# Kernel tuning notes

Hardware: AMD Instinct MI355X
Metric: run time of the kernel (lower is better)

## Reference

```python
import jax, jax.numpy as jnp
import numpy as np
import math

B, S, E, H = 2, 2048, 1024, 16
D = E // H
# neuromodulator levels (deterministic branch choices)
NA, ACH, DA = 0.5, 0.5, -0.5

def setup_inputs() -> dict:
    key = jax.random.key(0)
    ks = jax.random.split(key, 12)
    xav = lambda k, i, o: jax.random.uniform(k, (i, o), jnp.float32, -1.0, 1.0) * math.sqrt(6.0 / (i + o))
    return {
        'query': jax.random.normal(ks[0], (B, S, E), jnp.float32),
        'key':   jax.random.normal(ks[1], (B, S, E), jnp.float32),
        'value': jax.random.normal(ks[2], (B, S, E), jnp.float32),
        'Wq': xav(ks[3], E, E), 'bq': jnp.zeros((E,), jnp.float32),
        'Wk': xav(ks[4], E, E), 'bk': jnp.zeros((E,), jnp.float32),
        'Wv': xav(ks[5], E, E), 'bv': jnp.zeros((E,), jnp.float32),
        'Wo': xav(ks[6], E, E), 'bo': jnp.zeros((E,), jnp.float32),
        'time_scales': jnp.ones((H,), jnp.float32),
    }

def reference(query, key, value, Wq, bq, Wk, bk, Wv, bv, Wo, bo, time_scales):
    # projections -> [B, H, S, D]
    q = (query @ Wq + bq).reshape(B, S, H, D).transpose(0, 2, 1, 3)
    k = (key   @ Wk + bk).reshape(B, S, H, D).transpose(0, 2, 1, 3)
    v = (value @ Wv + bv).reshape(B, S, H, D).transpose(0, 2, 1, 3)
    # per-head time-scale on keys
    k = k * time_scales[None, :, None, None]
    scores = jnp.einsum('bhtd,bhsd->bhts', q, k) / math.sqrt(D)
    # noradrenaline: temperature scaling
    temperature = 1.0 / (1.0 + NA * 0.5)
    scores = scores / temperature
    # acetylcholine: boost diagonal
    diag = jnp.eye(S, dtype=scores.dtype)[None, None]
    scores = scores * (1.0 + ACH * 0.3 * diag)
    kk = max(1, int(S * 0.2))
    topv = jax.lax.top_k(scores, kk)[0]          # [B,H,S,kk]
    min_topk = topv[..., -1:]                     # kth largest
    mask = (scores >= min_topk).astype(scores.dtype)
    scores = scores * (1.0 + (-DA) * 0.3 * mask)
    attn = jax.nn.softmax(scores, axis=-1)
    out = jnp.einsum('bhts,bhsd->bhtd', attn, v)
    out = out.transpose(0, 2, 1, 3).reshape(B, S, E)
    out = out @ Wo + bo
    return out
```

## Files before the change

kernel.cpp:

```cpp
#include <hip/hip_runtime.h>
#include <cstdint>
#include <cstddef>

#define BB 2
#define SS 2048
#define EE 1024
#define HH 16
#define DH 64
#define KKSEL 409
#define QT 16
#define PST 136

typedef __attribute__((ext_vector_type(8))) short bf16x8;
typedef __attribute__((ext_vector_type(4))) float f32x4;
typedef unsigned short ushort_t;

__device__ __forceinline__ unsigned short f2bf(float f){
    unsigned u = __float_as_uint(f);
    u += 0x7fffu + ((u >> 16) & 1u);
    return (unsigned short)(u >> 16);
}
__device__ __forceinline__ float bf2f(unsigned short h){
    return __uint_as_float(((unsigned)h) << 16);
}
__device__ __forceinline__ unsigned sortkey(float f){
    unsigned u = __float_as_uint(f);
    return (u & 0x80000000u) ? ~u : (u | 0x80000000u);
}
__device__ __forceinline__ float inv_sortkey(unsigned k){
    unsigned u = (k & 0x80000000u) ? (k & 0x7fffffffu) : ~k;
    return __uint_as_float(u);
}
__device__ __forceinline__ void split8(const float* f, bf16x8& h, bf16x8& l){
    #pragma unroll
    for (int j = 0; j < 8; ++j){
        ushort_t hh = f2bf(f[j]);
        h[j] = (short)hh;
        l[j] = (short)f2bf(f[j] - bf2f(hh));
    }
}
__device__ __forceinline__ void gload_lds16(const ushort_t* g, ushort_t* l){
    __builtin_amdgcn_global_load_lds(
        (const __attribute__((address_space(1))) void*)g,
        (__attribute__((address_space(3))) void*)l, 16, 0, 0);
}

__device__ __forceinline__ float topk_thresh(const float* cand){
    float mx = cand[0], mn = cand[0];
    #pragma unroll
    for (int j = 1; j < 32; ++j){
        mx = fmaxf(mx, cand[j]);
        mn = fminf(mn, cand[j]);
    }
    #pragma unroll
    for (int off = 1; off < 64; off <<= 1){
        mx = fmaxf(mx, __shfl_xor(mx, off, 64));
        mn = fminf(mn, __shfl_xor(mn, off, 64));
    }
    unsigned lo = sortkey(mn), hi = sortkey(mx) + 1u;
    #pragma unroll 1
    for (int it = 0; it < 32 && (hi - lo) > 1u; ++it){
        const unsigned mid = lo + ((hi - lo) >> 1);
        const float midf = inv_sortkey(mid);
        int c = 0;
        #pragma unroll
        for (int j = 0; j < 32; ++j)
            c += (int)__popcll(__ballot(cand[j] >= midf));
        if (c == KKSEL){ lo = mid; break; }
        if (c > KKSEL) lo = mid; else hi = mid;
    }
    return inv_sortkey(lo);
}

struct CvtArgs {
    const float* W[4];
    ushort_t* H[4];
    ushort_t* L[4];
};

__global__ __launch_bounds__(256) void convert_wt4(CvtArgs a)
{
    __shared__ float T[64][65];
    const int z = blockIdx.z;
    const float* __restrict__ W = a.W[z];
    ushort_t* __restrict__ Ht = a.H[z];
    ushort_t* __restrict__ Lt = a.L[z];

    const int tid = threadIdx.x;
    const int ty = tid >> 4, tx = tid & 15;
    const int n0 = blockIdx.x * 64, k0 = blockIdx.y * 64;
    #pragma unroll
    for (int i = 0; i < 4; ++i){
        const int kl = ty + i * 16;
        float4 w = *(const float4*)&W[(size_t)(k0 + kl) * EE + n0 + tx * 4];
        T[kl][tx*4 + 0] = w.x; T[kl][tx*4 + 1] = w.y;
        T[kl][tx*4 + 2] = w.z; T[kl][tx*4 + 3] = w.w;
    }
    __syncthreads();
    #pragma unroll
    for (int i = 0; i < 4; ++i){
        const int nl = ty + i * 16;
        ushort4 h, l;
        ushort_t* hp = &h.x; ushort_t* lp = &l.x;
        #pragma unroll
        for (int j = 0; j < 4; ++j){
            const float v = T[tx*4 + j][nl];
            ushort_t hh = f2bf(v);
            hp[j] = hh;
            lp[j] = f2bf(v - bf2f(hh));
        }
        const size_t o = (size_t)(n0 + nl) * EE + k0 + tx * 4;
        *(ushort4*)&Ht[o] = h;
        *(ushort4*)&Lt[o] = l;
    }
}

template<int MODE>
__device__ __forceinline__ void gemm_body(
        const float* __restrict__ X,
        const ushort_t* __restrict__ Wth, const ushort_t* __restrict__ Wtl,
        const float* __restrict__ bias, const float* __restrict__ ts,
        float* __restrict__ OutF, ushort_t* __restrict__ OutH,
        ushort_t* __restrict__ OutL, ushort_t* buf)
{
    const int tid  = threadIdx.x;
    const int lane = tid & 63, wave = tid >> 6;
    const int c16  = lane & 15, qd = lane >> 4;
    const int m0 = blockIdx.y * 128, n0 = blockIdx.x * 128;
    const int wm = (wave >> 1) * 64, wn = (wave & 1) * 64;
    const int lrow = tid >> 1, lkg = (tid & 1) * 16;

    f32x4 acc[4][4];
    #pragma unroll
    for (int a = 0; a < 4; ++a)
        #pragma unroll
        for (int b = 0; b < 4; ++b) acc[a][b] = (f32x4){0.f,0.f,0.f,0.f};

    const float* Xr = X + (size_t)(m0 + lrow) * EE + lkg;

    const int seg0 = wave * 2, seg1 = wave * 2 + 1;
    const size_t wofs0 = (size_t)(n0 + seg0*16 + (lane >> 2)) * EE + (lane & 3) * 8;
    const size_t wofs1 = (size_t)(n0 + seg1*16 + (lane >> 2)) * EE + (lane & 3) * 8;
    const ushort_t* WhA = Wth + wofs0;
    const ushort_t* WhB = Wth + wofs1;
    const ushort_t* WlA = Wtl + wofs0;
    const ushort_t* WlB = Wtl + wofs1;

    {
        ushort_t* S = buf;
        gload_lds16(WhA, S + 8192  + seg0*512);
        gload_lds16(WhB, S + 8192  + seg1*512);
        gload_lds16(WlA, S + 12288 + seg0*512);
        gload_lds16(WlB, S + 12288 + seg1*512);
        float fx[16];
        *(float4*)&fx[0]  = *(const float4*)&Xr[0];
        *(float4*)&fx[4]  = *(const float4*)&Xr[4];
        *(float4*)&fx[8]  = *(const float4*)&Xr[8];
        *(float4*)&fx[12] = *(const float4*)&Xr[12];
        bf16x8 h0, l0, h1, l1;
        split8(fx, h0, l0); split8(fx + 8, h1, l1);
        *(bf16x8*)&S[lrow*32 + lkg]           = h0;
        *(bf16x8*)&S[lrow*32 + lkg + 8]       = h1;
        *(bf16x8*)&S[4096 + lrow*32 + lkg]    = l0;
        *(bf16x8*)&S[4096 + lrow*32 + lkg+8]  = l1;
    }
    __syncthreads();

    int cur = 0;
    for (int k0 = 0; k0 < EE; k0 += 32){
        const bool more = (k0 + 32) < EE;
        float fx[16];
        if (more){
            const int kt = k0 + 32;
            ushort_t* N = buf + (cur ^ 1) * 16384;
            gload_lds16(WhA + kt, N + 8192  + seg0*512);
            gload_lds16(WhB + kt, N + 8192  + seg1*512);
            gload_lds16(WlA + kt, N + 12288 + seg0*512);
            gload_lds16(WlB + kt, N + 12288 + seg1*512);
            const float* xp = Xr + kt;
            *(float4*)&fx[0]  = *(const float4*)&xp[0];
            *(float4*)&fx[4]  = *(const float4*)&xp[4];
            *(float4*)&fx[8]  = *(const float4*)&xp[8];
            *(float4*)&fx[12] = *(const float4*)&xp[12];
        }
        const ushort_t* S  = buf + cur * 16384;
        const ushort_t* A0 = S;
        const ushort_t* A1 = S + 4096;
        const ushort_t* B0 = S + 8192;
        const ushort_t* B1 = S + 12288;
        bf16x8 afh[4], afl[4], bfh[4], bfl[4];
        #pragma unroll
        for (int i = 0; i < 4; ++i){
            afh[i] = *(const bf16x8*)&A0[(wm + i*16 + c16)*32 + qd*8];
            afl[i] = *(const bf16x8*)&A1[(wm + i*16 + c16)*32 + qd*8];
            bfh[i] = *(const bf16x8*)&B0[(wn + i*16 + c16)*32 + qd*8];
            bfl[i] = *(const bf16x8*)&B1[(wn + i*16 + c16)*32 + qd*8];
        }
        #pragma unroll
        for (int a = 0; a < 4; ++a){
            #pragma unroll
            for (int b = 0; b < 4; ++b){
                if (MODE == 2){
                    acc[a][b] = __builtin_amdgcn_mfma_f32_16x16x32_bf16(afh[a], bfh[b], acc[a][b], 0,0,0);
                    acc[a][b] = __builtin_amdgcn_mfma_f32_16x16x32_bf16(afh[a], bfl[b], acc[a][b], 0,0,0);
                    acc[a][b] = __builtin_amdgcn_mfma_f32_16x16x32_bf16(afl[a], bfh[b], acc[a][b], 0,0,0);
                } else {
                    acc[a][b] = __builtin_amdgcn_mfma_f32_16x16x32_bf16(bfh[a], afh[b], acc[a][b], 0,0,0);
                    acc[a][b] = __builtin_amdgcn_mfma_f32_16x16x32_bf16(bfh[a], afl[b], acc[a][b], 0,0,0);
                    acc[a][b] = __builtin_amdgcn_mfma_f32_16x16x32_bf16(bfl[a], afh[b], acc[a][b], 0,0,0);
                }
            }
        }
        if (more){
            bf16x8 h0, l0, h1, l1;
            split8(fx, h0, l0); split8(fx + 8, h1, l1);
            ushort_t* N = buf + (cur ^ 1) * 16384;
            *(bf16x8*)&N[lrow*32 + lkg]           = h0;
            *(bf16x8*)&N[lrow*32 + lkg + 8]       = h1;
            *(bf16x8*)&N[4096 + lrow*32 + lkg]    = l0;
            *(bf16x8*)&N[4096 + lrow*32 + lkg+8]  = l1;
            __syncthreads();
            cur ^= 1;
        }
    }

    if (MODE == 3){
        #pragma unroll
        for (int a = 0; a < 4; ++a){
            const int ng = n0 + wn + a*16 + qd*4;
            float4 b4 = *(const float4*)&bias[ng];
            const float bb[4] = {b4.x, b4.y, b4.z, b4.w};
            #pragma unroll
            for (int b = 0; b < 4; ++b){
                const int mg = m0 + wm + b*16 + c16;
                float4 o;
                o.x = acc[a][b][0] + bb[0]; o.y = acc[a][b][1] + bb[1];
                o.z = acc[a][b][2] + bb[2]; o.w = acc[a][b][3] + bb[3];
                *(float4*)&OutF[(size_t)mg * EE + ng] = o;
            }
        }
    } else if (MODE == 0){
        #pragma unroll
        for (int a = 0; a < 4; ++a){
            const int ng = n0 + wn + a*16 + qd*4;
            const int h = ng >> 6, d0 = ng & 63;
            float4 b4 = *(const float4*)&bias[ng];
            const float bb[4] = {b4.x, b4.y, b4.z, b4.w};
            #pragma unroll
            for (int b = 0; b < 4; ++b){
                const int mg = m0 + wm + b*16 + c16;
                const int bi = mg >> 11, s = mg & (SS - 1);
                ushort4 hv, lv;
                ushort_t* hp = &hv.x; ushort_t* lp = &lv.x;
                #pragma unroll
                for (int r = 0; r < 4; ++r){
                    const float v = (acc[a][b][r] + bb[r]) * 0.15625f;
                    ushort_t hh = f2bf(v);
                    hp[r] = hh;
                    lp[r] = f2bf(v - bf2f(hh));
                }
                const size_t o = (((size_t)(bi * HH + h)) * SS + s) * DH + d0;
                *(ushort4*)&OutH[o] = hv;
                *(ushort4*)&OutL[o] = lv;
            }
        }
    } else if (MODE == 1){
        #pragma unroll
        for (int a = 0; a < 4; ++a){
            const int ng = n0 + wn + a*16 + qd*4;
            const int h = ng >> 6, d0 = ng & 63;
            const float tsc = ts[h];
            float4 b4 = *(const float4*)&bias[ng];
            const float bb[4] = {b4.x, b4.y, b4.z, b4.w};
            #pragma unroll
            for (int b = 0; b < 4; ++b){
                const int mg = m0 + wm + b*16 + c16;
                const int bi = mg >> 11, s = mg & (SS - 1);
                ushort4 hv;
                ushort_t* hp = &hv.x;
                #pragma unroll
                for (int r = 0; r < 4; ++r)
                    hp[r] = f2bf((acc[a][b][r] + bb[r]) * tsc);
                *(ushort4*)&OutH[(((size_t)(bi * HH + h)) * SS + s) * DH + d0] = hv;
            }
        }
    } else {
        #pragma unroll
        for (int a = 0; a < 4; ++a){
            const int mg = m0 + wm + a*16 + qd*4;
            const int bi = mg >> 11, s0 = mg & (SS - 1);
            #pragma unroll
            for (int b = 0; b < 4; ++b){
                const int ng = n0 + wn + b*16 + c16;
                const int h = ng >> 6, d = ng & 63;
                const float bv = bias[ng];
                ushort4 hv;
                ushort_t* hp = &hv.x;
                #pragma unroll
                for (int r = 0; r < 4; ++r) hp[r] = f2bf(acc[a][b][r] + bv);
                *(ushort4*)&OutH[(((size_t)(bi * HH + h)) * DH + d) * SS + s0] = hv;
            }
        }
    }
}

__global__ __launch_bounds__(256) void gemm_qkv(
        const float* __restrict__ q, const float* __restrict__ k,
        const float* __restrict__ v,
        const ushort_t* __restrict__ Wqh, const ushort_t* __restrict__ Wql,
        const ushort_t* __restrict__ Wkh, const ushort_t* __restrict__ Wkl,
        const ushort_t* __restrict__ Wvh, const ushort_t* __restrict__ Wvl,
        const float* __restrict__ bq, const float* __restrict__ bk,
        const float* __restrict__ bv, const float* __restrict__ ts,
        ushort_t* __restrict__ Qh, ushort_t* __restrict__ Ql,
        ushort_t* __restrict__ Kh, ushort_t* __restrict__ Vth)
{
    __shared__ ushort_t buf[2 * 16384];
    const int z = blockIdx.z;
    if (z == 0)
        gemm_body<0>(q, Wqh, Wql, bq, nullptr, nullptr, Qh, Ql, buf);
    else if (z == 1)
        gemm_body<1>(k, Wkh, Wkl, bk, ts, nullptr, Kh, nullptr, buf);
    else
        gemm_body<2>(v, Wvh, Wvl, bv, nullptr, nullptr, Vth, nullptr, buf);
}

__global__ __launch_bounds__(256) void gemm_out(
        const float* __restrict__ X,
        const ushort_t* __restrict__ Wth, const ushort_t* __restrict__ Wtl,
        const float* __restrict__ bias, float* __restrict__ OutF)
{
    __shared__ ushort_t buf[2 * 16384];
    gemm_body<3>(X, Wth, Wtl, bias, nullptr, OutF, nullptr, nullptr, buf);
}

__global__ __launch_bounds__(512, 4) void attn_kernel(
        const ushort_t* __restrict__ Qh, const ushort_t* __restrict__ Ql,
        const ushort_t* __restrict__ Khi, const ushort_t* __restrict__ Vth,
        float* __restrict__ AO)
{
    __shared__ __align__(16) char uni[65536];
    __shared__ float wsums[8][16];
    __shared__ float thr16[16];

    const int tid  = threadIdx.x;
    const int lane = tid & 63;
    const int wave = tid >> 6;
    const int qd   = lane >> 4;
    const int c16  = lane & 15;
    const unsigned Bx = blockIdx.x;
    const int xcd  = Bx & 7;
    const int qq   = Bx >> 3;
    const int tile = qq & 127;
    const int bh   = (qq >> 7) * 8 + xcd;
    const int t0   = tile * QT;
    const int wbase = wave * 256;

    bf16x8 qh[2], ql[2];
    {
        const size_t qbase = ((size_t)bh * SS + t0 + c16) * DH;
        #pragma unroll
        for (int kc = 0; kc < 2; ++kc){
            qh[kc] = *(const bf16x8*)&Qh[qbase + kc*32 + qd*8];
            ql[kc] = *(const bf16x8*)&Ql[qbase + kc*32 + qd*8];
        }
    }

    f32x4 acc[16];
    const ushort_t* Kh = Khi + (size_t)bh * SS * DH;
    #pragma unroll
    for (int t = 0; t < 16; ++t){
        f32x4 a = {0.f, 0.f, 0.f, 0.f};
        const int srow = wbase + t*16 + c16;
        const ushort_t* kp = Kh + (size_t)srow * DH + qd*8;
        #pragma unroll
        for (int kc = 0; kc < 2; ++kc){
            bf16x8 kh = *(const bf16x8*)(kp + kc*32);
            a = __builtin_amdgcn_mfma_f32_16x16x32_bf16(qh[kc], kh, a, 0, 0, 0);
            a = __builtin_amdgcn_mfma_f32_16x16x32_bf16(ql[kc], kh, a, 0, 0, 0);
        }
        acc[t] = a;
    }

    if (wave == (t0 >> 8)){
        #pragma unroll
        for (int t = 0; t < 16; ++t){
            const int colg = wbase + t*16 + c16;
            #pragma unroll
            for (int r = 0; r < 4; ++r)
                if (colg == t0 + qd*4 + r) acc[t][r] *= 1.15f;
        }
    }

    float* ex = (float*)uni;
    if (qd < 2){
        const int rl = (qd & 1) * 4;
        #pragma unroll
        for (int t = 0; t < 16; ++t)
            #pragma unroll
            for (int r = 0; r < 4; ++r)
                ex[(rl + r) * SS + wbase + t*16 + c16] = acc[t][r];
    }
    __syncthreads();
    float cand[32];
    #pragma unroll
    for (int j = 0; j < 32; ++j)
        cand[j] = ex[wave * SS + lane + 64*j];
    __syncthreads();
    if (qd >= 2){
        const int rl = (qd & 1) * 4;
        #pragma unroll
        for (int t = 0; t < 16; ++t)
            #pragma unroll
            for (int r = 0; r < 4; ++r)
                ex[(rl + r) * SS + wbase + t*16 + c16] = acc[t][r];
    }
    {
        const float th0 = topk_thresh(cand);
        if (lane == 0) thr16[wave] = th0;
    }
    __syncthreads();
    #pragma unroll
    for (int j = 0; j < 32; ++j)
        cand[j] = ex[wave * SS + lane + 64*j];
    {
        const float th1 = topk_thresh(cand);
        if (lane == 0) thr16[8 + wave] = th1;
    }
    __syncthreads();

    float thr[4];
    #pragma unroll
    for (int r = 0; r < 4; ++r) thr[r] = thr16[qd*4 + r];
    float psum[4] = {0.f, 0.f, 0.f, 0.f};
    #pragma unroll
    for (int t = 0; t < 16; ++t){
        #pragma unroll
        for (int r = 0; r < 4; ++r){
            const float s = acc[t][r];
            const float m = (s >= thr[r]) ? 1.15f : 1.0f;
            const float e = __expf(s * m);
            acc[t][r] = e;
            psum[r] += e;
        }
    }
    #pragma unroll
    for (int off = 1; off <= 8; off <<= 1){
        #pragma unroll
        for (int r = 0; r < 4; ++r) psum[r] += __shfl_xor(psum[r], off, 64);
    }
    if (c16 == 0){
        #pragma unroll
        for (int r = 0; r < 4; ++r) wsums[wave][qd*4 + r] = psum[r];
    }
    __syncthreads();
    float pinv[4];
    #pragma unroll
    for (int r = 0; r < 4; ++r){
        const int row = qd*4 + r;
        float s = 0.f;
        #pragma unroll
        for (int w = 0; w < 8; ++w) s += wsums[w][row];
        pinv[r] = 1.f / s;
    }

    const ushort_t* Vh = Vth + (size_t)bh * DH * SS;
    ushort_t* pw = (ushort_t*)uni + wave * (QT * PST);
    f32x4 oacc[4];
    #pragma unroll
    for (int dt = 0; dt < 4; ++dt) oacc[dt] = (f32x4){0.f, 0.f, 0.f, 0.f};

    #pragma unroll
    for (int half = 0; half < 2; ++half){
        #pragma unroll
        for (int tt = 0; tt < 8; ++tt){
            const int t = half*8 + tt;
            #pragma unroll
            for (int r = 0; r < 4; ++r)
                pw[(qd*4 + r) * PST + tt*16 + c16] = f2bf(acc[t][r] * pinv[r]);
        }
        #pragma unroll
        for (int kc = 0; kc < 4; ++kc){
            bf16x8 pf = *(const bf16x8*)&pw[c16 * PST + kc*32 + qd*8];
            const int sbase = wbase + half*128 + kc*32 + qd*8;
            #pragma unroll
            for (int dt = 0; dt < 4; ++dt){
                const int d = dt*16 + c16;
                bf16x8 vh = *(const bf16x8*)(Vh + (size_t)d * SS + sbase);
                oacc[dt] = __builtin_amdgcn_mfma_f32_16x16x32_bf16(pf, vh, oacc[dt], 0, 0, 0);
            }
        }
    }

    __syncthreads();
    float* red = (float*)uni;
    #pragma unroll
    for (int dt = 0; dt < 4; ++dt)
        #pragma unroll
        for (int r = 0; r < 4; ++r)
            red[(wave*16 + qd*4 + r) * 65 + dt*16 + c16] = oacc[dt][r];
    __syncthreads();

    const int b = bh >> 4, h = bh & 15;
    {
        const int r  = tid >> 5;
        const int c2 = (tid & 31) * 2;
        float s0 = 0.f, s1 = 0.f;
        #pragma unroll
        for (int w = 0; w < 8; ++w){
            s0 += red[(w*16 + r) * 65 + c2];
            s1 += red[(w*16 + r) * 65 + c2 + 1];
        }
        float2 o; o.x = s0; o.y = s1;
        *(float2*)&AO[((size_t)b * SS + t0 + r) * EE + h*DH + c2] = o;
    }
}

extern "C" void kernel_launch(void* const* d_in, const int* in_sizes, int n_in,
                              void* d_out, int out_size, void* d_ws, size_t ws_size,
                              hipStream_t stream)
{
    const float* query = (const float*)d_in[0];
    const float* key   = (const float*)d_in[1];
    const float* value = (const float*)d_in[2];
    const float* Wq    = (const float*)d_in[3];
    const float* bq    = (const float*)d_in[4];
    const float* Wk    = (const float*)d_in[5];
    const float* bk    = (const float*)d_in[6];
    const float* Wv    = (const float*)d_in[7];
    const float* bv    = (const float*)d_in[8];
    const float* Wo    = (const float*)d_in[9];
    const float* bo    = (const float*)d_in[10];
    const float* ts    = (const float*)d_in[11];
    float* out = (float*)d_out;
    char* w = (char*)d_ws;

    const size_t MB = 1u << 20;
    ushort_t* Qh  = (ushort_t*)(w + 0 * MB);
    ushort_t* Ql  = (ushort_t*)(w + 8 * MB);
    ushort_t* Kh  = (ushort_t*)(w + 16 * MB);
    ushort_t* Vth = (ushort_t*)(w + 24 * MB);
    float*    AOw = (float*)   (w + 32 * MB);
    ushort_t* Wqh = (ushort_t*)(w + 32 * MB);
    ushort_t* Wql = (ushort_t*)(w + 34 * MB);
    ushort_t* Wkh = (ushort_t*)(w + 36 * MB);
    ushort_t* Wkl = (ushort_t*)(w + 38 * MB);
    ushort_t* Wvh = (ushort_t*)(w + 40 * MB);
    ushort_t* Wvl = (ushort_t*)(w + 42 * MB);
    ushort_t* Woh = (ushort_t*)(w + 48 * MB);
    ushort_t* Wol = (ushort_t*)(w + 50 * MB);

    CvtArgs ca;
    ca.W[0] = Wq;  ca.W[1] = Wk;  ca.W[2] = Wv;  ca.W[3] = Wo;
    ca.H[0] = Wqh; ca.H[1] = Wkh; ca.H[2] = Wvh; ca.H[3] = Woh;
    ca.L[0] = Wql; ca.L[1] = Wkl; ca.L[2] = Wvl; ca.L[3] = Wol;

    hipLaunchKernelGGL(convert_wt4, dim3(16, 16, 4), dim3(256), 0, stream, ca);
    hipLaunchKernelGGL(gemm_qkv, dim3(8, 32, 3), dim3(256), 0, stream,
                       query, key, value, Wqh, Wql, Wkh, Wkl, Wvh, Wvl,
                       bq, bk, bv, ts, Qh, Ql, Kh, Vth);
    hipLaunchKernelGGL(attn_kernel, dim3(BB * HH * (SS / QT)), dim3(512), 0, stream,
                       Qh, Ql, Kh, Vth, AOw);
    hipLaunchKernelGGL(gemm_out, dim3(8, 32), dim3(256), 0, stream,
                       AOw, Woh, Wol, bo, out);
}
```

Baseline: 671.5 us.

## Pre-split activations to bf16 hi/lo and stage GEMM A tiles via direct LDS loads

```diff
diff --git a/kernel.cpp b/kernel.cpp
--- a/kernel.cpp
+++ b/kernel.cpp
@@ -45,8 +45,8 @@
         (__attribute__((address_space(3))) void*)l, 16, 0, 0);
 }
 
-__device__ __forceinline__ float topk_thresh(const float* cand){
-    float mx = cand[0], mn = cand[0];
+__device__ __forceinline__ void wave_minmax(const float* cand, float& mn, float& mx){
+    mx = cand[0]; mn = cand[0];
     #pragma unroll
     for (int j = 1; j < 32; ++j){
         mx = fmaxf(mx, cand[j]);
@@ -57,6 +57,8 @@
         mx = fmaxf(mx, __shfl_xor(mx, off, 64));
         mn = fminf(mn, __shfl_xor(mn, off, 64));
     }
+}
+__device__ __forceinline__ float bisect_thresh(const float* cand, float mn, float mx){
     unsigned lo = sortkey(mn), hi = sortkey(mx) + 1u;
     #pragma unroll 1
     for (int it = 0; it < 32 && (hi - lo) > 1u; ++it){
@@ -115,9 +117,31 @@
     }
 }
 
+struct CvtX {
+    const float* X[3];
+    ushort_t* H[3];
+    ushort_t* L[3];
+};
+
+__global__ __launch_bounds__(256) void convert_x3(CvtX a)
+{
+    const int z = blockIdx.z;
+    const float* __restrict__ X = a.X[z];
+    ushort_t* __restrict__ Hd = a.H[z];
+    ushort_t* __restrict__ Ld = a.L[z];
+    const size_t i = ((size_t)blockIdx.x * 256 + threadIdx.x) * 8;
+    float fx[8];
+    *(float4*)&fx[0] = *(const float4*)&X[i];
+    *(float4*)&fx[4] = *(const float4*)&X[i + 4];
+    bf16x8 h, l;
+    split8(fx, h, l);
+    *(bf16x8*)&Hd[i] = h;
+    *(bf16x8*)&Ld[i] = l;
+}
+
 template<int MODE>
 __device__ __forceinline__ void gemm_body(
-        const float* __restrict__ X,
+        const ushort_t* __restrict__ Xh, const ushort_t* __restrict__ Xl,
         const ushort_t* __restrict__ Wth, const ushort_t* __restrict__ Wtl,
         const float* __restrict__ bias, const float* __restrict__ ts,
         float* __restrict__ OutF, ushort_t* __restrict__ OutH,
@@ -128,7 +152,6 @@
     const int c16  = lane & 15, qd = lane >> 4;
     const int m0 = blockIdx.y * 128, n0 = blockIdx.x * 128;
     const int wm = (wave >> 1) * 64, wn = (wave & 1) * 64;
-    const int lrow = tid >> 1, lkg = (tid & 1) * 16;
 
     f32x4 acc[4][4];
     #pragma unroll
@@ -136,53 +159,31 @@
         #pragma unroll
         for (int b = 0; b < 4; ++b) acc[a][b] = (f32x4){0.f,0.f,0.f,0.f};
 
-    const float* Xr = X + (size_t)(m0 + lrow) * EE + lkg;
-
-    const int seg0 = wave * 2, seg1 = wave * 2 + 1;
-    const size_t wofs0 = (size_t)(n0 + seg0*16 + (lane >> 2)) * EE + (lane & 3) * 8;
-    const size_t wofs1 = (size_t)(n0 + seg1*16 + (lane >> 2)) * EE + (lane & 3) * 8;
-    const ushort_t* WhA = Wth + wofs0;
-    const ushort_t* WhB = Wth + wofs1;
-    const ushort_t* WlA = Wtl + wofs0;
-    const ushort_t* WlB = Wtl + wofs1;
-
-    {
-        ushort_t* S = buf;
-        gload_lds16(WhA, S + 8192  + seg0*512);
-        gload_lds16(WhB, S + 8192  + seg1*512);
-        gload_lds16(WlA, S + 12288 + seg0*512);
-        gload_lds16(WlB, S + 12288 + seg1*512);
-        float fx[16];
-        *(float4*)&fx[0]  = *(const float4*)&Xr[0];
-        *(float4*)&fx[4]  = *(const float4*)&Xr[4];
-        *(float4*)&fx[8]  = *(const float4*)&Xr[8];
-        *(float4*)&fx[12] = *(const float4*)&Xr[12];
-        bf16x8 h0, l0, h1, l1;
-        split8(fx, h0, l0); split8(fx + 8, h1, l1);
-        *(bf16x8*)&S[lrow*32 + lkg]           = h0;
-        *(bf16x8*)&S[lrow*32 + lkg + 8]       = h1;
-        *(bf16x8*)&S[4096 + lrow*32 + lkg]    = l0;
-        *(bf16x8*)&S[4096 + lrow*32 + lkg+8]  = l1;
-    }
+    const int seg0 = wave * 2, seg1 = seg0 + 1;
+    const int rl = lane >> 2, kl = (lane & 3) * 8;
+    const size_t aofs0 = (size_t)(m0 + seg0*16 + rl) * EE + kl;
+    const size_t aofs1 = (size_t)(m0 + seg1*16 + rl) * EE + kl;
+    const size_t bofs0 = (size_t)(n0 + seg0*16 + rl) * EE + kl;
+    const size_t bofs1 = (size_t)(n0 + seg1*16 + rl) * EE + kl;
+
+    auto stage = [&](ushort_t* S, int kt){
+        gload_lds16(Xh  + aofs0 + kt, S +         seg0*512);
+        gload_lds16(Xh  + aofs1 + kt, S +         seg1*512);
+        gload_lds16(Xl  + aofs0 + kt, S + 4096  + seg0*512);
+        gload_lds16(Xl  + aofs1 + kt, S + 4096  + seg1*512);
+        gload_lds16(Wth + bofs0 + kt, S + 8192  + seg0*512);
+        gload_lds16(Wth + bofs1 + kt, S + 8192  + seg1*512);
+        gload_lds16(Wtl + bofs0 + kt, S + 12288 + seg0*512);
+        gload_lds16(Wtl + bofs1 + kt, S + 12288 + seg1*512);
+    };
+
+    stage(buf, 0);
     __syncthreads();
 
     int cur = 0;
     for (int k0 = 0; k0 < EE; k0 += 32){
         const bool more = (k0 + 32) < EE;
-        float fx[16];
-        if (more){
-            const int kt = k0 + 32;
-            ushort_t* N = buf + (cur ^ 1) * 16384;
-            gload_lds16(WhA + kt, N + 8192  + seg0*512);
-            gload_lds16(WhB + kt, N + 8192  + seg1*512);
-            gload_lds16(WlA + kt, N + 12288 + seg0*512);
-            gload_lds16(WlB + kt, N + 12288 + seg1*512);
-            const float* xp = Xr + kt;
-            *(float4*)&fx[0]  = *(const float4*)&xp[0];
-            *(float4*)&fx[4]  = *(const float4*)&xp[4];
-            *(float4*)&fx[8]  = *(const float4*)&xp[8];
-            *(float4*)&fx[12] = *(const float4*)&xp[12];
-        }
+        if (more) stage(buf + (cur ^ 1) * 16384, k0 + 32);
         const ushort_t* S  = buf + cur * 16384;
         const ushort_t* A0 = S;
         const ushort_t* A1 = S + 4096;
@@ -212,13 +213,6 @@
             }
         }
         if (more){
-            bf16x8 h0, l0, h1, l1;
-            split8(fx, h0, l0); split8(fx + 8, h1, l1);
-            ushort_t* N = buf + (cur ^ 1) * 16384;
-            *(bf16x8*)&N[lrow*32 + lkg]           = h0;
-            *(bf16x8*)&N[lrow*32 + lkg + 8]       = h1;
-            *(bf16x8*)&N[4096 + lrow*32 + lkg]    = l0;
-            *(bf16x8*)&N[4096 + lrow*32 + lkg+8]  = l1;
             __syncthreads();
             cur ^= 1;
         }
@@ -305,8 +299,9 @@
 }
 
 __global__ __launch_bounds__(256) void gemm_qkv(
-        const float* __restrict__ q, const float* __restrict__ k,
-        const float* __restrict__ v,
+        const ushort_t* __restrict__ Xqh, const ushort_t* __restrict__ Xql,
+        const ushort_t* __restrict__ Xkh, const ushort_t* __restrict__ Xkl,
+        const ushort_t* __restrict__ Xvh, const ushort_t* __restrict__ Xvl,
         const ushort_t* __restrict__ Wqh, const ushort_t* __restrict__ Wql,
         const ushort_t* __restrict__ Wkh, const ushort_t* __restrict__ Wkl,
         const ushort_t* __restrict__ Wvh, const ushort_t* __restrict__ Wvl,
@@ -318,26 +313,26 @@
     __shared__ ushort_t buf[2 * 16384];
     const int z = blockIdx.z;
     if (z == 0)
-        gemm_body<0>(q, Wqh, Wql, bq, nullptr, nullptr, Qh, Ql, buf);
+        gemm_body<0>(Xqh, Xql, Wqh, Wql, bq, nullptr, nullptr, Qh, Ql, buf);
     else if (z == 1)
-        gemm_body<1>(k, Wkh, Wkl, bk, ts, nullptr, Kh, nullptr, buf);
+        gemm_body<1>(Xkh, Xkl, Wkh, Wkl, bk, ts, nullptr, Kh, nullptr, buf);
     else
-        gemm_body<2>(v, Wvh, Wvl, bv, nullptr, nullptr, Vth, nullptr, buf);
+        gemm_body<2>(Xvh, Xvl, Wvh, Wvl, bv, nullptr, nullptr, Vth, nullptr, buf);
 }
 
 __global__ __launch_bounds__(256) void gemm_out(
-        const float* __restrict__ X,
+        const ushort_t* __restrict__ AOh, const ushort_t* __restrict__ AOl,
         const ushort_t* __restrict__ Wth, const ushort_t* __restrict__ Wtl,
         const float* __restrict__ bias, float* __restrict__ OutF)
 {
     __shared__ ushort_t buf[2 * 16384];
-    gemm_body<3>(X, Wth, Wtl, bias, nullptr, OutF, nullptr, nullptr, buf);
+    gemm_body<3>(AOh, AOl, Wth, Wtl, bias, nullptr, OutF, nullptr, nullptr, buf);
 }
 
 __global__ __launch_bounds__(512, 4) void attn_kernel(
         const ushort_t* __restrict__ Qh, const ushort_t* __restrict__ Ql,
         const ushort_t* __restrict__ Khi, const ushort_t* __restrict__ Vth,
-        float* __restrict__ AO)
+        ushort_t* __restrict__ AOh, ushort_t* __restrict__ AOl)
 {
     __shared__ __align__(16) char uni[65536];
     __shared__ float wsums[8][16];
@@ -407,16 +402,18 @@
     for (int j = 0; j < 32; ++j)
         cand[j] = ex[wave * SS + lane + 64*j];
     __syncthreads();
-    if (qd >= 2){
-        const int rl = (qd & 1) * 4;
-        #pragma unroll
-        for (int t = 0; t < 16; ++t)
-            #pragma unroll
-            for (int r = 0; r < 4; ++r)
-                ex[(rl + r) * SS + wbase + t*16 + c16] = acc[t][r];
-    }
     {
-        const float th0 = topk_thresh(cand);
+        float mn, mx;
+        wave_minmax(cand, mn, mx);
+        if (qd >= 2){
+            const int rl = (qd & 1) * 4;
+            #pragma unroll
+            for (int t = 0; t < 16; ++t)
+                #pragma unroll
+                for (int r = 0; r < 4; ++r)
+                    ex[(rl + r) * SS + wbase + t*16 + c16] = acc[t][r];
+        }
+        const float th0 = bisect_thresh(cand, mn, mx);
         if (lane == 0) thr16[wave] = th0;
     }
     __syncthreads();
@@ -424,7 +421,9 @@
     for (int j = 0; j < 32; ++j)
         cand[j] = ex[wave * SS + lane + 64*j];
     {
-        const float th1 = topk_thresh(cand);
+        float mn, mx;
+        wave_minmax(cand, mn, mx);
+        const float th1 = bisect_thresh(cand, mn, mx);
         if (lane == 0) thr16[8 + wave] = th1;
     }
     __syncthreads();
@@ -466,29 +465,42 @@
 
     const ushort_t* Vh = Vth + (size_t)bh * DH * SS;
     ushort_t* pw = (ushort_t*)uni + wave * (QT * PST);
+
+    #pragma unroll
+    for (int tt = 0; tt < 8; ++tt)
+        #pragma unroll
+        for (int r = 0; r < 4; ++r)
+            pw[(qd*4 + r) * PST + tt*16 + c16] = f2bf(acc[tt][r] * pinv[r]);
+
     f32x4 oacc[4];
     #pragma unroll
     for (int dt = 0; dt < 4; ++dt) oacc[dt] = (f32x4){0.f, 0.f, 0.f, 0.f};
 
     #pragma unroll
-    for (int half = 0; half < 2; ++half){
-        #pragma unroll
-        for (int tt = 0; tt < 8; ++tt){
-            const int t = half*8 + tt;
-            #pragma unroll
-            for (int r = 0; r < 4; ++r)
-                pw[(qd*4 + r) * PST + tt*16 + c16] = f2bf(acc[t][r] * pinv[r]);
-        }
-        #pragma unroll
-        for (int kc = 0; kc < 4; ++kc){
-            bf16x8 pf = *(const bf16x8*)&pw[c16 * PST + kc*32 + qd*8];
-            const int sbase = wbase + half*128 + kc*32 + qd*8;
-            #pragma unroll
-            for (int dt = 0; dt < 4; ++dt){
-                const int d = dt*16 + c16;
-                bf16x8 vh = *(const bf16x8*)(Vh + (size_t)d * SS + sbase);
-                oacc[dt] = __builtin_amdgcn_mfma_f32_16x16x32_bf16(pf, vh, oacc[dt], 0, 0, 0);
-            }
+    for (int kc = 0; kc < 4; ++kc){
+        bf16x8 pf = *(const bf16x8*)&pw[c16 * PST + kc*32 + qd*8];
+        const int sbase = wbase + kc*32 + qd*8;
+        #pragma unroll
+        for (int dt = 0; dt < 4; ++dt){
+            const int d = dt*16 + c16;
+            bf16x8 vh = *(const bf16x8*)(Vh + (size_t)d * SS + sbase);
+            oacc[dt] = __builtin_amdgcn_mfma_f32_16x16x32_bf16(pf, vh, oacc[dt], 0, 0, 0);
+        }
+    }
+    #pragma unroll
+    for (int tt = 0; tt < 8; ++tt)
+        #pragma unroll
+        for (int r = 0; r < 4; ++r)
+            pw[(qd*4 + r) * PST + tt*16 + c16] = f2bf(acc[8 + tt][r] * pinv[r]);
+    #pragma unroll
+    for (int kc = 0; kc < 4; ++kc){
+        bf16x8 pf = *(const bf16x8*)&pw[c16 * PST + kc*32 + qd*8];
+        const int sbase = wbase + 128 + kc*32 + qd*8;
+        #pragma unroll
+        for (int dt = 0; dt < 4; ++dt){
+            const int d = dt*16 + c16;
+            bf16x8 vh = *(const bf16x8*)(Vh + (size_t)d * SS + sbase);
+            oacc[dt] = __builtin_amdgcn_mfma_f32_16x16x32_bf16(pf, vh, oacc[dt], 0, 0, 0);
         }
     }
 
@@ -511,8 +523,12 @@
             s0 += red[(w*16 + r) * 65 + c2];
             s1 += red[(w*16 + r) * 65 + c2 + 1];
         }
-        float2 o; o.x = s0; o.y = s1;
-        *(float2*)&AO[((size_t)b * SS + t0 + r) * EE + h*DH + c2] = o;
+        const size_t o = ((size_t)b * SS + t0 + r) * EE + h*DH + c2;
+        ushort2 hv, lv;
+        hv.x = f2bf(s0); lv.x = f2bf(s0 - bf2f(hv.x));
+        hv.y = f2bf(s1); lv.y = f2bf(s1 - bf2f(hv.y));
+        *(ushort2*)&AOh[o] = hv;
+        *(ushort2*)&AOl[o] = lv;
     }
 }
 
@@ -540,27 +556,41 @@
     ushort_t* Ql  = (ushort_t*)(w + 8 * MB);
     ushort_t* Kh  = (ushort_t*)(w + 16 * MB);
     ushort_t* Vth = (ushort_t*)(w + 24 * MB);
-    float*    AOw = (float*)   (w + 32 * MB);
     ushort_t* Wqh = (ushort_t*)(w + 32 * MB);
     ushort_t* Wql = (ushort_t*)(w + 34 * MB);
     ushort_t* Wkh = (ushort_t*)(w + 36 * MB);
     ushort_t* Wkl = (ushort_t*)(w + 38 * MB);
     ushort_t* Wvh = (ushort_t*)(w + 40 * MB);
     ushort_t* Wvl = (ushort_t*)(w + 42 * MB);
-    ushort_t* Woh = (ushort_t*)(w + 48 * MB);
-    ushort_t* Wol = (ushort_t*)(w + 50 * MB);
+    ushort_t* Woh = (ushort_t*)(w + 44 * MB);
+    ushort_t* Wol = (ushort_t*)(w + 46 * MB);
+    ushort_t* Xqh = (ushort_t*)(w + 48 * MB);
+    ushort_t* Xql = (ushort_t*)(w + 56 * MB);
+    ushort_t* Xkh = (ushort_t*)(w + 64 * MB);
+    ushort_t* Xkl = (ushort_t*)(w + 72 * MB);
+    ushort_t* Xvh = (ushort_t*)(w + 80 * MB);
+    ushort_t* Xvl = (ushort_t*)(w + 88 * MB);
+    ushort_t* AOh = (ushort_t*)(w + 48 * MB);
+    ushort_t* AOl = (ushort_t*)(w + 56 * MB);
 
     CvtArgs ca;
     ca.W[0] = Wq;  ca.W[1] = Wk;  ca.W[2] = Wv;  ca.W[3] = Wo;
     ca.H[0] = Wqh; ca.H[1] = Wkh; ca.H[2] = Wvh; ca.H[3] = Woh;
     ca.L[0] = Wql; ca.L[1] = Wkl; ca.L[2] = Wvl; ca.L[3] = Wol;
 
+    CvtX cx;
+    cx.X[0] = query; cx.X[1] = key; cx.X[2] = value;
+    cx.H[0] = Xqh;   cx.H[1] = Xkh; cx.H[2] = Xvh;
+    cx.L[0] = Xql;   cx.L[1] = Xkl; cx.L[2] = Xvl;
+
     hipLaunchKernelGGL(convert_wt4, dim3(16, 16, 4), dim3(256), 0, stream, ca);
+    hipLaunchKernelGGL(convert_x3, dim3(2048, 1, 3), dim3(256), 0, stream, cx);
     hipLaunchKernelGGL(gemm_qkv, dim3(8, 32, 3), dim3(256), 0, stream,
-                       query, key, value, Wqh, Wql, Wkh, Wkl, Wvh, Wvl,
+                       Xqh, Xql, Xkh, Xkl, Xvh, Xvl,
+                       Wqh, Wql, Wkh, Wkl, Wvh, Wvl,
                        bq, bk, bv, ts, Qh, Ql, Kh, Vth);
     hipLaunchKernelGGL(attn_kernel, dim3(BB * HH * (SS / QT)), dim3(512), 0, stream,
-                       Qh, Ql, Kh, Vth, AOw);
+                       Qh, Ql, Kh, Vth, AOh, AOl);
     hipLaunchKernelGGL(gemm_out, dim3(8, 32), dim3(256), 0, stream,
-                       AOw, Woh, Wol, bo, out);
-}
+                       AOh, AOl, Woh, Wol, bo, out);
+}
```

Result: slower. 694.8 us (+3.5%).
